# Kernel optimization log

Hardware: AMD Instinct MI355X
Metric: run time of the kernel (lower is better)

Reference implementation:

```python
import jax, jax.numpy as jnp
import numpy as np

N_NODES = 50000
N_EDGES = 1_600_000
IN_DIM = 128
OUT_DIM = 32
HEADS = 4
EDGE_DIM = 16


def setup_inputs() -> dict:
    key = jax.random.key(0)
    ks = jax.random.split(key, 8)
    x = jax.random.normal(ks[0], (N_NODES, IN_DIM), dtype=jnp.float32)
    edge_index = jax.random.randint(ks[1], (2, N_EDGES), 0, N_NODES, dtype=jnp.int32)
    edge_attr = jax.random.normal(ks[2], (N_EDGES, EDGE_DIM), dtype=jnp.float32)
    # parameters (xavier-ish small scale)
    W_lin = jax.random.normal(ks[3], (OUT_DIM * HEADS, IN_DIM), dtype=jnp.float32) * 0.08
    att_src = jax.random.normal(ks[4], (HEADS, OUT_DIM), dtype=jnp.float32) * 0.1
    att_dst = jax.random.normal(ks[5], (HEADS, OUT_DIM), dtype=jnp.float32) * 0.1
    bias = jnp.zeros((OUT_DIM,), dtype=jnp.float32)
    W_edge = jax.random.normal(ks[6], (HEADS, EDGE_DIM), dtype=jnp.float32) * 0.2
    return {"x": x, "edge_index": edge_index, "edge_attr": edge_attr,
            "W_lin": W_lin, "att_src": att_src, "att_dst": att_dst,
            "bias": bias, "W_edge": W_edge}


def reference(x, edge_index, edge_attr, W_lin, att_src, att_dst, bias, W_edge):
    num_nodes = x.shape[0]
    heads, out_dim = att_src.shape
    # h = lin(x) -> [N, H, D]
    h = (x @ W_lin.T).reshape(num_nodes, heads, out_dim)
    # per-node attention terms [N, H]
    a_src = jnp.einsum("nhd,hd->nh", h, att_src)
    a_dst = jnp.einsum("nhd,hd->nh", h, att_dst)
    src, dst = edge_index[0], edge_index[1]
    # edge logits [E, H]
    logits = a_src[src] + a_dst[dst] + edge_attr @ W_edge.T
    logits = jax.nn.leaky_relu(logits, negative_slope=0.2)
    # segment softmax over edges grouped by dst (vectorized across heads)
    max_vals = jax.ops.segment_max(logits, dst, num_segments=num_nodes)  # [N, H]
    exp_s = jnp.exp(logits - max_vals[dst])
    denom = jax.ops.segment_sum(exp_s, dst, num_segments=num_nodes)  # [N, H]
    alpha = exp_s / (denom[dst] + 1e-16)  # [E, H]
    # weighted aggregation: sum_e h[src_e] * alpha_e into dst nodes
    out = h[src] * alpha[:, :, None]  # [E, H, D]
    agg = jax.ops.segment_sum(out, dst, num_segments=num_nodes)  # [N, H, D]
    return agg.mean(axis=1) + bias
```

## Files before the change

kernel.cpp:

```cpp
#include <hip/hip_runtime.h>
#include <hip/hip_fp16.h>

#define N_NODES 50000
#define N_EDGES 1600000
#define IN_DIM  128
#define OUT_DIM 32
#define HEADS   4
#define EDGE_DIM 16

#define NB   512
#define DPB  98
#define CAP  4224
#define SC_CHUNK 1024
#define SC_EPT   4
#define PAD_DL 255
#define GC(b) ((b) * 16)

__global__ __launch_bounds__(256) void k_gemm(
    const float* __restrict__ x, const float* __restrict__ Wl,
    const float* __restrict__ att_src, const float* __restrict__ att_dst,
    __half* __restrict__ h2t, float* __restrict__ a_src,
    float* __restrict__ a_dst) {
  __shared__ float Wt[IN_DIM][68];
  __shared__ float attS[IN_DIM], attD[IN_DIM];
  __shared__ float sred_s[32][4], sred_d[32][4];
  const int t = threadIdx.x;
  const int n0 = blockIdx.x * 32;

  if (t < IN_DIM) { attS[t] = att_src[t]; attD[t] = att_dst[t]; }

  const int tx = t & 15, ty = t >> 4;
  const int na = n0 + 2 * ty, nb = na + 1;
  const float* xa_ptr = x + (size_t)((na < N_NODES) ? na : 0) * IN_DIM;
  const float* xb_ptr = x + (size_t)((nb < N_NODES) ? nb : 0) * IN_DIM;

  for (int p = 0; p < 2; ++p) {
    __syncthreads();
    for (int it = 0; it < 32; ++it) {
      int idx = it * 256 + t;
      int kg = (idx >> 7) + p * 64, i = idx & 127;
      Wt[i][kg - p * 64] = Wl[(size_t)kg * IN_DIM + i];
    }
    __syncthreads();

    float4 acc0 = {0.f,0.f,0.f,0.f}, acc1 = {0.f,0.f,0.f,0.f};
    #pragma unroll 4
    for (int i4 = 0; i4 < IN_DIM; i4 += 4) {
      float4 xa = *(const float4*)(xa_ptr + i4);
      float4 xb = *(const float4*)(xb_ptr + i4);
      const float* xap = (const float*)&xa;
      const float* xbp = (const float*)&xb;
      #pragma unroll
      for (int ii = 0; ii < 4; ++ii) {
        float4 wv = *(const float4*)&Wt[i4+ii][tx*4];
        float a = xap[ii], b = xbp[ii];
        acc0.x += a*wv.x; acc0.y += a*wv.y; acc0.z += a*wv.z; acc0.w += a*wv.w;
        acc1.x += b*wv.x; acc1.y += b*wv.y; acc1.z += b*wv.z; acc1.w += b*wv.w;
      }
    }
    const int k = p*64 + tx*4;
    const int hd = k >> 5, d0 = k & 31;
    const float* ap = (const float*)&acc0;
    const float* bp = (const float*)&acc1;

    float sa = ap[0]*attS[k] + ap[1]*attS[k+1] + ap[2]*attS[k+2] + ap[3]*attS[k+3];
    float da = ap[0]*attD[k] + ap[1]*attD[k+1] + ap[2]*attD[k+2] + ap[3]*attD[k+3];
    float sb = bp[0]*attS[k] + bp[1]*attS[k+1] + bp[2]*attS[k+2] + bp[3]*attS[k+3];
    float db = bp[0]*attD[k] + bp[1]*attD[k+1] + bp[2]*attD[k+2] + bp[3]*attD[k+3];
    #pragma unroll
    for (int off = 1; off <= 4; off <<= 1) {
      sa += __shfl_xor(sa, off); da += __shfl_xor(da, off);
      sb += __shfl_xor(sb, off); db += __shfl_xor(db, off);
    }
    if ((tx & 7) == 0) {
      sred_s[2*ty][hd] = sa; sred_s[2*ty+1][hd] = sb;
      sred_d[2*ty][hd] = da; sred_d[2*ty+1][hd] = db;
    }

    if (na < N_NODES) {
      #pragma unroll
      for (int j = 0; j < 4; ++j)
        h2t[(size_t)na*IN_DIM + (d0+j)*4 + hd] = __float2half(ap[j]);
    }
    if (nb < N_NODES) {
      #pragma unroll
      for (int j = 0; j < 4; ++j)
        h2t[(size_t)nb*IN_DIM + (d0+j)*4 + hd] = __float2half(bp[j]);
    }
  }
  __syncthreads();
  if (t < 128) {
    int node = t >> 2;
    if (n0 + node < N_NODES)
      a_src[(size_t)(n0 + node) * 4 + (t & 3)] = sred_s[node][t & 3];
  } else {
    int tt = t - 128, node = tt >> 2;
    if (n0 + node < N_NODES)
      a_dst[(size_t)(n0 + node) * 4 + (tt & 3)] = sred_d[node][tt & 3];
  }
}

__global__ __launch_bounds__(256) void k_scatter3(
    const int* __restrict__ ei, const float* __restrict__ eattr,
    const float* __restrict__ a_src, const float* __restrict__ a_dst,
    const float* __restrict__ W_edge, unsigned int* __restrict__ gcursor,
    float4* __restrict__ rec) {
  __shared__ float We[HEADS * EDGE_DIM];
  __shared__ unsigned int cntb[NB], gbase[NB];
  const int t = threadIdx.x;
  if (t < HEADS * EDGE_DIM) We[t] = W_edge[t];
  for (int i = t; i < NB; i += 256) cntb[i] = 0u;
  __syncthreads();

  const int base = blockIdx.x * SC_CHUNK;
  unsigned int rx[SC_EPT], ry[SC_EPT], rz[SC_EPT], rk[SC_EPT];
  int bk[SC_EPT]; unsigned char dl8[SC_EPT]; bool ok[SC_EPT];

  #pragma unroll
  for (int i = 0; i < SC_EPT; ++i) {
    int e = base + i * 256 + t;
    ok[i] = (e < N_EDGES);
    if (ok[i]) {
      int src = ei[e], dst = ei[N_EDGES + e];
      float asp[4], adp[4], ea[EDGE_DIM];
      *(float4*)asp = *(const float4*)(a_src + (size_t)src * 4);
      *(float4*)adp = *(const float4*)(a_dst + (size_t)dst * 4);
      #pragma unroll
      for (int j = 0; j < 4; ++j)
        *(float4*)&ea[j*4] = *(const float4*)(eattr + (size_t)e * EDGE_DIM + j*4);
      float pv[HEADS];
      #pragma unroll
      for (int hh = 0; hh < HEADS; ++hh) {
        float sum = asp[hh] + adp[hh];
        #pragma unroll
        for (int j = 0; j < EDGE_DIM; ++j) sum += ea[j] * We[hh*EDGE_DIM + j];
        float lg = (sum > 0.f) ? sum : 0.2f * sum;
        pv[hh] = __expf(lg);
      }
      __half2 p01 = __floats2half2_rn(pv[0], pv[1]);
      __half2 p23 = __floats2half2_rn(pv[2], pv[3]);
      int b = dst / DPB;
      bk[i] = b;
      dl8[i] = (unsigned char)(dst - b * DPB);
      rx[i] = *(const unsigned int*)&p01;
      ry[i] = *(const unsigned int*)&p23;
      rz[i] = (unsigned int)src;
      rk[i] = atomicAdd(&cntb[b], 1u);
    }
  }
  __syncthreads();

  for (int b = t; b < NB; b += 256) {
    unsigned int c = cntb[b];
    if (c) {
      unsigned int creq = (c + 1u) & ~1u;
      unsigned int gb = atomicAdd(&gcursor[GC(b)], creq);
      gbase[b] = gb;
      if ((c & 1u) && (gb + c < CAP)) {
        float4 z;
        z.x = 0.f; z.y = 0.f; z.z = 0.f;
        z.w = __uint_as_float((unsigned int)PAD_DL);
        rec[(size_t)b * CAP + gb + c] = z;
      }
    }
  }
  __syncthreads();

  #pragma unroll
  for (int i = 0; i < SC_EPT; ++i) {
    if (ok[i]) {
      unsigned int pos = gbase[bk[i]] + rk[i];
      if (pos < CAP) {
        float4 r;
        r.x = __uint_as_float(rx[i]); r.y = __uint_as_float(ry[i]);
        r.z = __uint_as_float(rz[i]); r.w = __uint_as_float((unsigned int)dl8[i]);
        rec[(size_t)bk[i] * CAP + pos] = r;
      }
    }
  }
}

__global__ __launch_bounds__(1024) void k_bagg(
    const unsigned int* __restrict__ gcursor, const float4* __restrict__ rec,
    const __half* __restrict__ h2t, const float* __restrict__ bias,
    float* __restrict__ out) {
  __shared__ float4 srec[CAP];
  __shared__ unsigned short idx[CAP];
  __shared__ unsigned int cnt[256], off[256], cnt2[256];
  const int t = threadIdx.x;
  const int b = blockIdx.x;
  const size_t base = (size_t)b * CAP;
  unsigned int cntT = gcursor[GC(b)];
  if (cntT > CAP) cntT = CAP;

  if (t < 256) { cnt[t] = 0u; cnt2[t] = 0u; }
  __syncthreads();

  int dl_r[5]; unsigned short jj[5]; int nmine = 0;
  for (unsigned int j = t; j < cntT; j += 1024) {
    float4 r = rec[base + j];
    srec[j] = r;
    int dl = (int)__float_as_uint(r.w);
    dl_r[nmine] = dl; jj[nmine] = (unsigned short)j; ++nmine;
    atomicAdd(&cnt[dl], 1u);
  }
  __syncthreads();
  if (t == 0) {
    unsigned int run = 0;
    for (int i = 0; i < 256; ++i) { off[i] = run; run += cnt[i]; }
  }
  __syncthreads();
  for (int k = 0; k < nmine; ++k) {
    int dl = dl_r[k];
    if (dl != PAD_DL) {
      unsigned int r = atomicAdd(&cnt2[dl], 1u);
      idx[off[dl] + r] = jj[k];
    }
  }
  __syncthreads();

  const int wv = t >> 6, lane = t & 63, half_ = lane >> 5, dd = lane & 31;
  for (int dl = wv; dl < DPB; dl += 16) {
    int node = b * DPB + dl;
    if (node >= N_NODES) break;
    const unsigned int s0 = off[dl], c = cnt[dl];

    float acc0 = 0.f, acc1 = 0.f, acc2 = 0.f, acc3 = 0.f;
    float dn0 = 0.f, dn1 = 0.f, dn2 = 0.f, dn3 = 0.f;

    unsigned int j = half_;
    for (; j + 2 < c; j += 4) {
      float4 ra = srec[idx[s0 + j]];
      float4 rb = srec[idx[s0 + j + 2]];
      unsigned int a01 = __float_as_uint(ra.x), a23 = __float_as_uint(ra.y);
      unsigned int b01 = __float_as_uint(rb.x), b23 = __float_as_uint(rb.y);
      int sa = (int)__float_as_uint(ra.z), sb = (int)__float_as_uint(rb.z);
      uint2 hra = *(const uint2*)(h2t + (size_t)sa * IN_DIM + dd * 4);
      uint2 hrb = *(const uint2*)(h2t + (size_t)sb * IN_DIM + dd * 4);
      float2 pa01 = __half22float2(*(const __half2*)&a01);
      float2 pa23 = __half22float2(*(const __half2*)&a23);
      dn0 += pa01.x; dn1 += pa01.y; dn2 += pa23.x; dn3 += pa23.y;
      float2 ha01 = __half22float2(*(const __half2*)&hra.x);
      float2 ha23 = __half22float2(*(const __half2*)&hra.y);
      acc0 += pa01.x * ha01.x; acc1 += pa01.y * ha01.y;
      acc2 += pa23.x * ha23.x; acc3 += pa23.y * ha23.y;
      float2 pb01 = __half22float2(*(const __half2*)&b01);
      float2 pb23 = __half22float2(*(const __half2*)&b23);
      dn0 += pb01.x; dn1 += pb01.y; dn2 += pb23.x; dn3 += pb23.y;
      float2 hb01 = __half22float2(*(const __half2*)&hrb.x);
      float2 hb23 = __half22float2(*(const __half2*)&hrb.y);
      acc0 += pb01.x * hb01.x; acc1 += pb01.y * hb01.y;
      acc2 += pb23.x * hb23.x; acc3 += pb23.y * hb23.y;
    }
    for (; j < c; j += 2) {
      float4 r = srec[idx[s0 + j]];
      unsigned int u01 = __float_as_uint(r.x), u23 = __float_as_uint(r.y);
      int src = (int)__float_as_uint(r.z);
      uint2 raw = *(const uint2*)(h2t + (size_t)src * IN_DIM + dd * 4);
      float2 p01 = __half22float2(*(const __half2*)&u01);
      float2 p23 = __half22float2(*(const __half2*)&u23);
      dn0 += p01.x; dn1 += p01.y; dn2 += p23.x; dn3 += p23.y;
      float2 h01 = __half22float2(*(const __half2*)&raw.x);
      float2 h23 = __half22float2(*(const __half2*)&raw.y);
      acc0 += p01.x * h01.x; acc1 += p01.y * h01.y;
      acc2 += p23.x * h23.x; acc3 += p23.y * h23.y;
    }

    dn0 += __shfl_xor(dn0, 32); dn1 += __shfl_xor(dn1, 32);
    dn2 += __shfl_xor(dn2, 32); dn3 += __shfl_xor(dn3, 32);
    acc0 += __shfl_xor(acc0, 32); acc1 += __shfl_xor(acc1, 32);
    acc2 += __shfl_xor(acc2, 32); acc3 += __shfl_xor(acc3, 32);

    if (half_ == 0) {
      float v = acc0 * (0.25f / (dn0 + 1e-16f)) + acc1 * (0.25f / (dn1 + 1e-16f))
              + acc2 * (0.25f / (dn2 + 1e-16f)) + acc3 * (0.25f / (dn3 + 1e-16f));
      out[(size_t)node * OUT_DIM + dd] = v + bias[dd];
    }
  }
}

extern "C" void kernel_launch(void* const* d_in, const int* in_sizes, int n_in,
                              void* d_out, int out_size, void* d_ws, size_t ws_size,
                              hipStream_t stream) {
  const float* x       = (const float*)d_in[0];
  const int*   ei      = (const int*)d_in[1];
  const float* eattr   = (const float*)d_in[2];
  const float* W_lin   = (const float*)d_in[3];
  const float* att_src = (const float*)d_in[4];
  const float* att_dst = (const float*)d_in[5];
  const float* bias    = (const float*)d_in[6];
  const float* W_edge  = (const float*)d_in[7];
  float* out = (float*)d_out;

  __half* h2t  = (__half*)d_ws;
  float4* rec  = (float4*)(h2t + (size_t)N_NODES * IN_DIM);
  float* a_src = (float*)(rec + (size_t)NB * CAP);
  float* a_dst = a_src + (size_t)N_NODES * HEADS;
  unsigned int* gcursor = (unsigned int*)(a_dst + (size_t)N_NODES * HEADS);

  hipMemsetAsync(gcursor, 0, (size_t)NB * 16 * sizeof(unsigned int), stream);

  k_gemm<<<(N_NODES + 31) / 32, 256, 0, stream>>>(
      x, W_lin, att_src, att_dst, h2t, a_src, a_dst);
  k_scatter3<<<(N_EDGES + SC_CHUNK - 1) / SC_CHUNK, 256, 0, stream>>>(
      ei, eattr, a_src, a_dst, W_edge, gcursor, rec);
  k_bagg<<<NB, 1024, 0, stream>>>(gcursor, rec, h2t, bias, out);
}
```

Measured before the change: 181.6 us.

## Batch scatter loads ahead of compute and pack global cursors densely

Restructures the scatter kernel so all gather loads (indices, a_src/a_dst rows, edge attributes) for the thread's four edges are issued up front before any compute, increasing memory-level parallelism. It adds a launch-bounds occupancy hint. It also removes the 64-byte padding between the per-bucket global cursors, shrinking the memset but putting several cursors in one cache line, where their atomics may contend.

```diff
diff --git a/kernel.cpp b/kernel.cpp
--- a/kernel.cpp
+++ b/kernel.cpp
@@ -14,7 +14,6 @@
 #define SC_CHUNK 1024
 #define SC_EPT   4
 #define PAD_DL 255
-#define GC(b) ((b) * 16)
 
 __global__ __launch_bounds__(256) void k_gemm(
     const float* __restrict__ x, const float* __restrict__ Wl,
@@ -100,7 +99,7 @@
   }
 }
 
-__global__ __launch_bounds__(256) void k_scatter3(
+__global__ __launch_bounds__(256, 2) void k_scatter3(
     const int* __restrict__ ei, const float* __restrict__ eattr,
     const float* __restrict__ a_src, const float* __restrict__ a_dst,
     const float* __restrict__ W_edge, unsigned int* __restrict__ gcursor,
@@ -113,40 +112,50 @@
   __syncthreads();
 
   const int base = blockIdx.x * SC_CHUNK;
-  unsigned int rx[SC_EPT], ry[SC_EPT], rz[SC_EPT], rk[SC_EPT];
-  int bk[SC_EPT]; unsigned char dl8[SC_EPT]; bool ok[SC_EPT];
-
+
+  int src[SC_EPT], dstv[SC_EPT]; bool ok[SC_EPT];
+  float4 as[SC_EPT], ad[SC_EPT];
+  float4 ea0[SC_EPT], ea1[SC_EPT], ea2[SC_EPT], ea3[SC_EPT];
   #pragma unroll
   for (int i = 0; i < SC_EPT; ++i) {
     int e = base + i * 256 + t;
     ok[i] = (e < N_EDGES);
-    if (ok[i]) {
-      int src = ei[e], dst = ei[N_EDGES + e];
-      float asp[4], adp[4], ea[EDGE_DIM];
-      *(float4*)asp = *(const float4*)(a_src + (size_t)src * 4);
-      *(float4*)adp = *(const float4*)(a_dst + (size_t)dst * 4);
+    int s = ok[i] ? ei[e] : 0;
+    int d = ok[i] ? ei[N_EDGES + e] : 0;
+    src[i] = s; dstv[i] = d;
+    as[i] = *(const float4*)(a_src + (size_t)s * 4);
+    ad[i] = *(const float4*)(a_dst + (size_t)d * 4);
+    const float4* ep = (const float4*)(eattr + (size_t)e * EDGE_DIM);
+    if (ok[i]) { ea0[i] = ep[0]; ea1[i] = ep[1]; ea2[i] = ep[2]; ea3[i] = ep[3]; }
+  }
+
+  unsigned int rx[SC_EPT], ry[SC_EPT], rk[SC_EPT];
+  int bk[SC_EPT]; unsigned char dl8[SC_EPT];
+  #pragma unroll
+  for (int i = 0; i < SC_EPT; ++i) {
+    if (!ok[i]) continue;
+    float ea[EDGE_DIM];
+    *(float4*)&ea[0]  = ea0[i]; *(float4*)&ea[4]  = ea1[i];
+    *(float4*)&ea[8]  = ea2[i]; *(float4*)&ea[12] = ea3[i];
+    const float* asp = (const float*)&as[i];
+    const float* adp = (const float*)&ad[i];
+    float pv[HEADS];
+    #pragma unroll
+    for (int hh = 0; hh < HEADS; ++hh) {
+      float sum = asp[hh] + adp[hh];
       #pragma unroll
-      for (int j = 0; j < 4; ++j)
-        *(float4*)&ea[j*4] = *(const float4*)(eattr + (size_t)e * EDGE_DIM + j*4);
-      float pv[HEADS];
-      #pragma unroll
-      for (int hh = 0; hh < HEADS; ++hh) {
-        float sum = asp[hh] + adp[hh];
-        #pragma unroll
-        for (int j = 0; j < EDGE_DIM; ++j) sum += ea[j] * We[hh*EDGE_DIM + j];
-        float lg = (sum > 0.f) ? sum : 0.2f * sum;
-        pv[hh] = __expf(lg);
-      }
-      __half2 p01 = __floats2half2_rn(pv[0], pv[1]);
-      __half2 p23 = __floats2half2_rn(pv[2], pv[3]);
-      int b = dst / DPB;
-      bk[i] = b;
-      dl8[i] = (unsigned char)(dst - b * DPB);
-      rx[i] = *(const unsigned int*)&p01;
-      ry[i] = *(const unsigned int*)&p23;
-      rz[i] = (unsigned int)src;
-      rk[i] = atomicAdd(&cntb[b], 1u);
-    }
+      for (int j = 0; j < EDGE_DIM; ++j) sum += ea[j] * We[hh*EDGE_DIM + j];
+      float lg = (sum > 0.f) ? sum : 0.2f * sum;
+      pv[hh] = __expf(lg);
+    }
+    __half2 p01 = __floats2half2_rn(pv[0], pv[1]);
+    __half2 p23 = __floats2half2_rn(pv[2], pv[3]);
+    int b = dstv[i] / DPB;
+    bk[i] = b;
+    dl8[i] = (unsigned char)(dstv[i] - b * DPB);
+    rx[i] = *(const unsigned int*)&p01;
+    ry[i] = *(const unsigned int*)&p23;
+    rk[i] = atomicAdd(&cntb[b], 1u);
   }
   __syncthreads();
 
@@ -154,7 +163,7 @@
     unsigned int c = cntb[b];
     if (c) {
       unsigned int creq = (c + 1u) & ~1u;
-      unsigned int gb = atomicAdd(&gcursor[GC(b)], creq);
+      unsigned int gb = atomicAdd(&gcursor[b], creq);
       gbase[b] = gb;
       if ((c & 1u) && (gb + c < CAP)) {
         float4 z;
@@ -173,7 +182,8 @@
       if (pos < CAP) {
         float4 r;
         r.x = __uint_as_float(rx[i]); r.y = __uint_as_float(ry[i]);
-        r.z = __uint_as_float(rz[i]); r.w = __uint_as_float((unsigned int)dl8[i]);
+        r.z = __uint_as_float((unsigned int)src[i]);
+        r.w = __uint_as_float((unsigned int)dl8[i]);
         rec[(size_t)bk[i] * CAP + pos] = r;
       }
     }
@@ -190,7 +200,7 @@
   const int t = threadIdx.x;
   const int b = blockIdx.x;
   const size_t base = (size_t)b * CAP;
-  unsigned int cntT = gcursor[GC(b)];
+  unsigned int cntT = gcursor[b];
   if (cntT > CAP) cntT = CAP;
 
   if (t < 256) { cnt[t] = 0u; cnt2[t] = 0u; }
@@ -298,7 +308,7 @@
   float* a_dst = a_src + (size_t)N_NODES * HEADS;
   unsigned int* gcursor = (unsigned int*)(a_dst + (size_t)N_NODES * HEADS);
 
-  hipMemsetAsync(gcursor, 0, (size_t)NB * 16 * sizeof(unsigned int), stream);
+  hipMemsetAsync(gcursor, 0, (size_t)NB * sizeof(unsigned int), stream);
 
   k_gemm<<<(N_NODES + 31) / 32, 256, 0, stream>>>(
       x, W_lin, att_src, att_dst, h2t, a_src, a_dst);
```

Result: faster. 165.1 us, median of 2 (-9.1%).
